# Optimization experiments

Hardware: AMD Instinct MI355X
Metric: run time of the kernel (lower is better)

## Reference

```python
import jax, jax.numpy as jnp
import numpy as np
from math import sqrt

B, N, CS, H, D, K = 8, 256, 512, 8, 64, 32
NB = 2 * K + 1          # no_bins = 65
CT = 2048               # c_transition
INF = 1e9
WL = sqrt(0.5)          # w_L
EPS = 1e-5


def setup_inputs() -> dict:
    key = jax.random.key(0)
    ks = jax.random.split(key, 10)
    sc = 0.02
    return {
        "s": jax.random.normal(ks[0], (B, N, CS), jnp.float32),
        "masks": jnp.ones((B, N), jnp.bool_),
        "wq": jax.random.normal(ks[1], (CS, D * H), jnp.float32) * sc,
        "wk": jax.random.normal(ks[2], (CS, D * H), jnp.float32) * sc,
        "wv": jax.random.normal(ks[3], (CS, D * H), jnp.float32) * sc,
        "wb": jax.random.normal(ks[4], (NB, H), jnp.float32) * sc,
        "wo": jax.random.normal(ks[5], ((NB + D) * H, CS), jnp.float32) * sc,
        "bo": jnp.zeros((CS,), jnp.float32),
        "ln1_g": jnp.ones((CS,), jnp.float32),
        "ln1_b": jnp.zeros((CS,), jnp.float32),
        "w1": jax.random.normal(ks[6], (CS, CT), jnp.float32) * sc,
        "b1": jnp.zeros((CT,), jnp.float32),
        "w2": jax.random.normal(ks[7], (CT, CS), jnp.float32) * sc,
        "b2": jnp.zeros((CS,), jnp.float32),
        "ln2_g": jnp.ones((CS,), jnp.float32),
        "ln2_b": jnp.zeros((CS,), jnp.float32),
    }


def _layernorm(x, g, b):
    m = jnp.mean(x, -1, keepdims=True)
    v = jnp.var(x, -1, keepdims=True)
    return (x - m) * jax.lax.rsqrt(v + EPS) * g + b


def _heads(x):  # [B,N,D*H] -> [B,H,N,D]  (torch: reshape(B,N,D,H) then move H forward)
    return jnp.transpose(x.reshape(B, N, D, H), (0, 3, 1, 2))


def reference(s, masks, wq, wk, wv, wb, wo, bo, ln1_g, ln1_b, w1, b1, w2, b2, ln2_g, ln2_b):
    mf = masks.astype(s.dtype)                       # [B,N]
    sq = mf[:, :, None] * mf[:, None, :]             # [B,N,N]

    # relative position one-hot, clipped to [-K, K] -> [N,N,NB]
    r = jnp.arange(N)
    dmat = jnp.clip(r[:, None] - r[None, :], -K, K) + K
    relpos_base = jax.nn.one_hot(dmat, NB, dtype=s.dtype)
    relpos = relpos_base[None] * sq[..., None]       # [B,N,N,NB]

    b_bias = jnp.einsum('bijc,ch->bhij', relpos, wb)  # [B,H,N,N]

    q = _heads(s @ wq)                               # [B,H,N,D]
    k = _heads(s @ wk)
    v = _heads(s @ wv)

    logits = WL * (jnp.einsum('bhid,bhjd->bhij', q, k) / sqrt(D) + b_bias)
    logits = logits - INF * (1.0 - sq)[:, None]      # mask
    a = jax.nn.softmax(logits, axis=-1)              # [B,H,N,N]

    # pairwise aggregation and value aggregation (einsum avoids [B,H,N,N,NB] blowup)
    o_pair = jnp.einsum('bhij,bijc->bhic', a, relpos)  # [B,H,N,NB]
    o = jnp.einsum('bhij,bhjd->bhid', a, v)            # [B,H,N,D]

    op = jnp.transpose(o_pair, (0, 2, 1, 3)).reshape(B, N, H * NB)
    ov = jnp.transpose(o, (0, 2, 1, 3)).reshape(B, N, H * D)
    embd = jnp.concatenate([op, ov], axis=-1) @ wo + bo   # [B,N,CS]

    x = _layernorm(s + embd, ln1_g, ln1_b)
    ff = jax.nn.relu(x @ w1 + b1) @ w2 + b2
    x = _layernorm(x + ff, ln2_g, ln2_b)
    return x, a
```

## Files before the change

### kernel.cpp

```cpp
#include <hip/hip_runtime.h>
#include <hip/hip_bf16.h>
#include <cstdint>

#define B_ 8
#define N_ 256
#define CS_ 512
#define H_ 8
#define D_ 64
#define K_ 32
#define NB_ 65
#define CT_ 2048
#define WL_ 0.70710678118654752f

typedef __attribute__((ext_vector_type(8))) short bf16x8;
typedef __attribute__((ext_vector_type(4))) float f32x4;

#define GLOBAL_AS __attribute__((address_space(1)))
#define LDS_AS __attribute__((address_space(3)))

__device__ __forceinline__ void async16(void* lds, const void* g) {
  __builtin_amdgcn_global_load_lds((const GLOBAL_AS uint32_t*)g,
                                   (LDS_AS uint32_t*)lds, 16, 0, 0);
}

__device__ __forceinline__ ushort f2bf(float v) {
  __hip_bfloat16 hb = __float2bfloat16(v);
  return *(ushort*)&hb;
}

__device__ __forceinline__ float bf2f(ushort u) {
  union { uint32_t ui; float f; } cv; cv.ui = (uint32_t)u << 16;
  return cv.f;
}

__global__ __launch_bounds__(128, 2) void gemm_bf16(
    const ushort* __restrict__ A, const ushort* __restrict__ Bt,
    const float* __restrict__ bias, float* __restrict__ C,
    ushort* __restrict__ Cb, int M, int Nc, int Kd, int flags) {
  __shared__ ushort As[2][64 * 64];
  __shared__ ushort Bs[2][64 * 64];
  int tid = threadIdx.x;
  int bm = blockIdx.y * 64, bn = blockIdx.x * 64;
  int S = gridDim.z, z = blockIdx.z;
  int T = Kd >> 6;
  int it0 = (z * T) / S, it1 = ((z + 1) * T) / S;
  if (flags & 32) Cb += (size_t)z * M * Nc;
  int w = tid >> 6, l = tid & 63;
  int lm = l & 15, lq = l >> 4;
  int srow = tid >> 3;
  int sg = tid & 7;

  f32x4 acc[2][4];
#pragma unroll
  for (int i = 0; i < 2; ++i)
#pragma unroll
    for (int j = 0; j < 4; ++j) acc[i][j] = (f32x4){0.f, 0.f, 0.f, 0.f};

  {
    int k0 = it0 << 6;
#pragma unroll
    for (int r = 0; r < 4; ++r) {
      int row = r * 16 + srow;
      int gl = sg ^ (row & 7);
      async16(&As[0][row * 64 + sg * 8],
              A + (size_t)(bm + row) * Kd + k0 + gl * 8);
      async16(&Bs[0][row * 64 + sg * 8],
              Bt + (size_t)(bn + row) * Kd + k0 + gl * 8);
    }
  }
  for (int it = it0; it < it1; ++it) {
    int cur = (it - it0) & 1;
    __syncthreads();
    if (it + 1 < it1) {
      int nxt = cur ^ 1;
      int k0 = (it + 1) << 6;
#pragma unroll
      for (int r = 0; r < 4; ++r) {
        int row = r * 16 + srow;
        int gl = sg ^ (row & 7);
        async16(&As[nxt][row * 64 + sg * 8],
                A + (size_t)(bm + row) * Kd + k0 + gl * 8);
        async16(&Bs[nxt][row * 64 + sg * 8],
                Bt + (size_t)(bn + row) * Kd + k0 + gl * 8);
      }
    }
#pragma unroll
    for (int kk = 0; kk < 2; ++kk) {
      bf16x8 af[2], bfr[4];
#pragma unroll
      for (int i = 0; i < 2; ++i) {
        int ma = w * 32 + 16 * i + lm;
        af[i] = *(const bf16x8*)&As[cur][ma * 64 + ((kk * 4 + lq) ^ (ma & 7)) * 8];
      }
#pragma unroll
      for (int j = 0; j < 4; ++j) {
        int nb = 16 * j + lm;
        bfr[j] = *(const bf16x8*)&Bs[cur][nb * 64 + ((kk * 4 + lq) ^ (nb & 7)) * 8];
      }
#pragma unroll
      for (int i = 0; i < 2; ++i)
#pragma unroll
        for (int j = 0; j < 4; ++j)
          acc[i][j] = __builtin_amdgcn_mfma_f32_16x16x32_bf16(
              af[i], bfr[j], acc[i][j], 0, 0, 0);
    }
  }
  __syncthreads();

  int lr = l >> 3, lc = l & 7;
  ushort* Tb = &As[0][0] + w * 2048;

#pragma unroll
  for (int j = 0; j < 4; ++j) {
    float bv = ((flags & 1) && z == 0) ? bias[bn + 16 * j + lm] : 0.f;
#pragma unroll
    for (int i = 0; i < 2; ++i)
#pragma unroll
      for (int r = 0; r < 4; ++r) {
        float v = acc[i][j][r] + bv;
        if (flags & 2) v = fmaxf(v, 0.f);
        Tb[(16 * i + lq * 4 + r) * 64 + 16 * j + lm] = f2bf(v);
      }
  }
  __asm__ __volatile__("" ::: "memory");
#pragma unroll
  for (int p = 0; p < 4; ++p) {
    int rowL = p * 8 + lr;
    bf16x8 vv = *(const bf16x8*)&Tb[rowL * 64 + lc * 8];
    *(bf16x8*)(Cb + (size_t)(bm + w * 32 + rowL) * Nc + bn + lc * 8) = vv;
  }
}

__global__ __launch_bounds__(128, 2) void qkvT(
    const ushort* __restrict__ A, const ushort* __restrict__ Bt,
    ushort* __restrict__ Cb,
    const float* __restrict__ wo, const float* __restrict__ w1,
    const float* __restrict__ w2, ushort* __restrict__ wopT,
    ushort* __restrict__ w1T, ushort* __restrict__ w2T) {
  __shared__ __align__(16) ushort As[2][64 * 64];
  __shared__ ushort Bs[2][64 * 64];
  int blk = blockIdx.x, tid = threadIdx.x;

  if (blk >= 768) {
    float (*tile)[33] = (float(*)[33])&As[0][0];
    int t = blk - 768;
    const float* src; ushort* dst;
    int R, C, Kpad, tX, tIdx;
    if (t < 544)       { tIdx = t;        src = wo; dst = wopT; R = 1032; C = 512;  Kpad = 1088; tX = 16; }
    else if (t < 1568) { tIdx = t - 544;  src = w1; dst = w1T;  R = 512;  C = 2048; Kpad = 512;  tX = 64; }
    else               { tIdx = t - 1568; src = w2; dst = w2T;  R = 2048; C = 512;  Kpad = 2048; tX = 16; }
    int c0 = (tIdx % tX) * 32, r0 = (tIdx / tX) * 32;
    int tx = tid & 7, ty = tid >> 3;
#pragma unroll
    for (int yy = 0; yy < 32; yy += 16) {
      int r = r0 + yy + ty, c = c0 + tx * 4;
      float4 v = (r < R) ? *(const float4*)&src[(size_t)r * C + c]
                         : (float4){0.f, 0.f, 0.f, 0.f};
      tile[yy + ty][tx * 4 + 0] = v.x;
      tile[yy + ty][tx * 4 + 1] = v.y;
      tile[yy + ty][tx * 4 + 2] = v.z;
      tile[yy + ty][tx * 4 + 3] = v.w;
    }
    __syncthreads();
#pragma unroll
    for (int yy = 0; yy < 32; yy += 16) {
      int cc = c0 + yy + ty;
      int k = r0 + tx * 4;
      float a0 = tile[tx * 4 + 0][yy + ty];
      float a1 = tile[tx * 4 + 1][yy + ty];
      float a2 = tile[tx * 4 + 2][yy + ty];
      float a3 = tile[tx * 4 + 3][yy + ty];
      ushort pk[4] = {f2bf(a0), f2bf(a1), f2bf(a2), f2bf(a3)};
      *(uint2*)&dst[(size_t)cc * Kpad + k] = *(uint2*)pk;
    }
    return;
  }

  int bm = (blk / 24) * 64, bn = (blk % 24) * 64;
  const int Kd = 512, it1 = 8;
  int w = tid >> 6, l = tid & 63;
  int lm = l & 15, lq = l >> 4;
  int srow = tid >> 3;
  int sg = tid & 7;

  f32x4 acc[2][4];
#pragma unroll
  for (int i = 0; i < 2; ++i)
#pragma unroll
    for (int j = 0; j < 4; ++j) acc[i][j] = (f32x4){0.f, 0.f, 0.f, 0.f};

  {
#pragma unroll
    for (int r = 0; r < 4; ++r) {
      int row = r * 16 + srow;
      int gl = sg ^ (row & 7);
      async16(&As[0][row * 64 + sg * 8],
              A + (size_t)(bm + row) * Kd + gl * 8);
      async16(&Bs[0][row * 64 + sg * 8],
              Bt + (size_t)(bn + row) * Kd + gl * 8);
    }
  }
  for (int it = 0; it < it1; ++it) {
    int cur = it & 1;
    __syncthreads();
    if (it + 1 < it1) {
      int nxt = cur ^ 1;
      int k0 = (it + 1) << 6;
#pragma unroll
      for (int r = 0; r < 4; ++r) {
        int row = r * 16 + srow;
        int gl = sg ^ (row & 7);
        async16(&As[nxt][row * 64 + sg * 8],
                A + (size_t)(bm + row) * Kd + k0 + gl * 8);
        async16(&Bs[nxt][row * 64 + sg * 8],
                Bt + (size_t)(bn + row) * Kd + k0 + gl * 8);
      }
    }
#pragma unroll
    for (int kk = 0; kk < 2; ++kk) {
      bf16x8 af[2], bfr[4];
#pragma unroll
      for (int i = 0; i < 2; ++i) {
        int ma = w * 32 + 16 * i + lm;
        af[i] = *(const bf16x8*)&As[cur][ma * 64 + ((kk * 4 + lq) ^ (ma & 7)) * 8];
      }
#pragma unroll
      for (int j = 0; j < 4; ++j) {
        int nb = 16 * j + lm;
        bfr[j] = *(const bf16x8*)&Bs[cur][nb * 64 + ((kk * 4 + lq) ^ (nb & 7)) * 8];
      }
#pragma unroll
      for (int i = 0; i < 2; ++i)
#pragma unroll
        for (int j = 0; j < 4; ++j)
          acc[i][j] = __builtin_amdgcn_mfma_f32_16x16x32_bf16(
              af[i], bfr[j], acc[i][j], 0, 0, 0);
    }
  }
  __syncthreads();

  int lr = l >> 3, lc = l & 7;
  ushort* Tb = &As[0][0] + w * 2048;

  int which = bn >> 9;
  int hh = (bn & 511) >> 6;
  int b = bm >> 8, nn0 = bm & 255;
  if (which == 2) {
#pragma unroll
    for (int j = 0; j < 4; ++j)
#pragma unroll
      for (int i = 0; i < 2; ++i) {
        ushort pk[4];
#pragma unroll
        for (int r = 0; r < 4; ++r) pk[r] = f2bf(acc[i][j][r]);
        *(uint2*)&Tb[(16 * j + lm) * 32 + 16 * i + lq * 4] = *(uint2*)pk;
      }
  } else {
#pragma unroll
    for (int j = 0; j < 4; ++j)
#pragma unroll
      for (int i = 0; i < 2; ++i)
#pragma unroll
        for (int r = 0; r < 4; ++r)
          Tb[(16 * i + lq * 4 + r) * 64 + 16 * j + lm] = f2bf(acc[i][j][r]);
  }
  __asm__ __volatile__("" ::: "memory");
  ushort* dstb = Cb + (size_t)which * 1048576 + (size_t)(b * 8 + hh) * 16384;
  if (which == 2) {
    int vr = l >> 2, vc = l & 3;
#pragma unroll
    for (int p = 0; p < 4; ++p) {
      int rowL = p * 16 + vr;
      bf16x8 vv = *(const bf16x8*)&Tb[rowL * 32 + vc * 8];
      *(bf16x8*)(dstb + (size_t)rowL * 256 + nn0 + w * 32 + vc * 8) = vv;
    }
  } else {
#pragma unroll
    for (int p = 0; p < 4; ++p) {
      int rowL = p * 8 + lr;
      bf16x8 vv = *(const bf16x8*)&Tb[rowL * 64 + lc * 8];
      *(bf16x8*)(dstb + (size_t)(nn0 + w * 32 + rowL) * 64 + lc * 8) = vv;
    }
  }
}

__global__ __launch_bounds__(256) void prep_small(
    const float* __restrict__ s, __hip_bfloat16* __restrict__ s_bf,
    const float* __restrict__ wq, const float* __restrict__ wk,
    const float* __restrict__ wv, __hip_bfloat16* __restrict__ wqkvT) {
  int blk = blockIdx.x;
  if (blk < 512) {
    int i = blk * 256 + threadIdx.x;
    float4 a = ((const float4*)s)[i * 2];
    float4 c = ((const float4*)s)[i * 2 + 1];
    ushort pk[8] = {f2bf(a.x), f2bf(a.y), f2bf(a.z), f2bf(a.w),
                    f2bf(c.x), f2bf(c.y), f2bf(c.z), f2bf(c.w)};
    *(uint4*)&((ushort*)s_bf)[i * 8] = *(uint4*)pk;
    return;
  }
  int t = blk - 512;
  __shared__ float tile[32][33];
  int zz = t >> 8, tIdx = t & 255;
  const float* src = zz == 0 ? wq : zz == 1 ? wk : wv;
  int whichBase = zz * 512;
  int c0 = (tIdx & 15) * 32, r0 = (tIdx >> 4) * 32;
  int tx = threadIdx.x & 7, ty = threadIdx.x >> 3;
  {
    int r = r0 + ty, c = c0 + tx * 4;
    float4 v = *(const float4*)&src[(size_t)r * 512 + c];
    tile[ty][tx * 4 + 0] = v.x;
    tile[ty][tx * 4 + 1] = v.y;
    tile[ty][tx * 4 + 2] = v.z;
    tile[ty][tx * 4 + 3] = v.w;
  }
  __syncthreads();
  {
    int cc = c0 + ty;
    int k = r0 + tx * 4;
    float a0 = tile[tx * 4 + 0][ty];
    float a1 = tile[tx * 4 + 1][ty];
    float a2 = tile[tx * 4 + 2][ty];
    float a3 = tile[tx * 4 + 3][ty];
    int n = whichBase + (cc & 7) * 64 + (cc >> 3);
    ushort pk[4] = {f2bf(a0), f2bf(a1), f2bf(a2), f2bf(a3)};
    *(uint2*)&((ushort*)wqkvT)[(size_t)n * 512 + k] = *(uint2*)pk;
  }
}

__global__ __launch_bounds__(128) void attn_fused(
    const ushort* __restrict__ qh, const ushort* __restrict__ kh,
    const ushort* __restrict__ vT, const int* __restrict__ masks,
    const float* __restrict__ wb, float* __restrict__ a_out,
    ushort* __restrict__ cat) {
  int strip = blockIdx.x & 7, bh = blockIdx.x >> 3;
  int h = bh & 7, b = bh >> 3;
  __shared__ ushort Ks[256 * 64];
  __shared__ ushort Ps[32 * 64];
  __shared__ float wbs[NB_];
  __shared__ float mfj[256];
  int tid = threadIdx.x;
  int srow = tid >> 3, sg = tid & 7;
#pragma unroll
  for (int rr = 0; rr < 16; ++rr) {
    int row = rr * 16 + srow;
    int gl = sg ^ (row & 7);
    async16(&Ks[row * 64 + sg * 8],
            kh + ((size_t)bh * 256 + row) * 64 + gl * 8);
  }
  int w = tid >> 6, l = tid & 63, lm = l & 15, lq = l >> 4;
  bf16x8 qf[2];
  {
    const ushort* qrow =
        qh + ((size_t)bh * 256 + strip * 32 + w * 16 + lm) * 64 + lq * 8;
    qf[0] = *(const bf16x8*)qrow;
    qf[1] = *(const bf16x8*)(qrow + 32);
  }
  if (tid < NB_) wbs[tid] = wb[tid * H_ + h];
  mfj[tid]       = (masks[b * 256 + tid] != 0) ? 1.f : 0.f;
  mfj[tid + 128] = (masks[b * 256 + tid + 128] != 0) ? 1.f : 0.f;
  __syncthreads();

  f32x4 acc[16];
#pragma unroll
  for (int ct = 0; ct < 16; ++ct) {
    int krow = ct * 16 + lm;
    bf16x8 kf0 = *(const bf16x8*)&Ks[krow * 64 + ((lq) ^ (krow & 7)) * 8];
    bf16x8 kf1 = *(const bf16x8*)&Ks[krow * 64 + ((4 + lq) ^ (krow & 7)) * 8];
    f32x4 zf = (f32x4){0.f, 0.f, 0.f, 0.f};
    zf = __builtin_amdgcn_mfma_f32_16x16x32_bf16(qf[0], kf0, zf, 0, 0, 0);
    acc[ct] = __builtin_amdgcn_mfma_f32_16x16x32_bf16(qf[1], kf1, zf, 0, 0, 0);
  }
  int ibase = strip * 32 + w * 16 + lq * 4;
  float mfi[4];
#pragma unroll
  for (int r = 0; r < 4; ++r) mfi[r] = mfj[ibase + r];
#pragma unroll
  for (int ct = 0; ct < 16; ++ct) {
    int j = ct * 16 + lm;
    float mj = mfj[j];
#pragma unroll
    for (int r = 0; r < 4; ++r) {
      int i = ibase + r;
      int diff = i - j;
      int cb = diff < -K_ ? 0 : (diff > K_ ? 2 * K_ : diff + K_);
      float sq = mfi[r] * mj;
      acc[ct][r] = WL_ * (acc[ct][r] * 0.125f + wbs[cb] * sq) - 1e9f * (1.f - sq);
    }
  }
  float mx[4], sm[4];
#pragma unroll
  for (int r = 0; r < 4; ++r) {
    float m = acc[0][r];
#pragma unroll
    for (int ct = 1; ct < 16; ++ct) m = fmaxf(m, acc[ct][r]);
#pragma unroll
    for (int o = 1; o < 16; o <<= 1) m = fmaxf(m, __shfl_xor(m, o, 64));
    mx[r] = m;
  }
#pragma unroll
  for (int ct = 0; ct < 16; ++ct)
#pragma unroll
    for (int r = 0; r < 4; ++r) acc[ct][r] = __expf(acc[ct][r] - mx[r]);
#pragma unroll
  for (int r = 0; r < 4; ++r) {
    float s = 0.f;
#pragma unroll
    for (int ct = 0; ct < 16; ++ct) s += acc[ct][r];
#pragma unroll
    for (int o = 1; o < 16; o <<= 1) s += __shfl_xor(s, o, 64);
    sm[r] = 1.f / s;
  }
  float p0[4] = {0.f, 0.f, 0.f, 0.f}, p64[4] = {0.f, 0.f, 0.f, 0.f};
#pragma unroll
  for (int ct = 0; ct < 16; ++ct) {
    int j = ct * 16 + lm;
    float mj = mfj[j];
#pragma unroll
    for (int r = 0; r < 4; ++r) {
      int i = ibase + r;
      float aval = acc[ct][r] * sm[r];
      a_out[((size_t)bh * 256 + i) * 256 + j] = aval;
      float val = aval * mfi[r] * mj;
      int diff = i - j;
      if (diff <= -K_)      p0[r] += val;
      else if (diff >= K_)  p64[r] += val;
      else cat[((size_t)(b * 256 + i)) * 1088 + h * 65 + diff + K_] = f2bf(val);
    }
  }
#pragma unroll
  for (int r = 0; r < 4; ++r)
#pragma unroll
    for (int o = 1; o < 16; o <<= 1) {
      p0[r]  += __shfl_xor(p0[r], o, 64);
      p64[r] += __shfl_xor(p64[r], o, 64);
    }
  if (lm == 0) {
#pragma unroll
    for (int r = 0; r < 4; ++r) {
      int i = ibase + r;
      cat[((size_t)(b * 256 + i)) * 1088 + h * 65 + 0]      = f2bf(p0[r]);
      cat[((size_t)(b * 256 + i)) * 1088 + h * 65 + 2 * K_] = f2bf(p64[r]);
    }
  }
#pragma unroll
  for (int r = 0; r < 4; ++r) {
    int i = ibase + r;
#pragma unroll
    for (int t = 0; t < 4; ++t) {
      int c = 1 + lm + 16 * t;
      if (c < 64) {
        int j = i - c + K_;
        if (j < 0 || j > 255)
          cat[((size_t)(b * 256 + i)) * 1088 + h * 65 + c] = 0;
      }
    }
  }
  if (h == 0) {
    for (int idx = tid; idx < 32 * 56; idx += 128) {
      int r = idx / 56, c = 1032 + (idx - r * 56);
      cat[((size_t)(b * 256 + strip * 32 + r)) * 1088 + c] = 0;
    }
  }
  f32x4 acc2[4];
#pragma unroll
  for (int nt = 0; nt < 4; ++nt) acc2[nt] = (f32x4){0.f, 0.f, 0.f, 0.f};
  const ushort* vbase = vT + (size_t)bh * 16384;
#pragma unroll
  for (int qt = 0; qt < 4; ++qt) {
    bf16x8 vf0[4], vf1[4];
#pragma unroll
    for (int nt = 0; nt < 4; ++nt) {
      const ushort* vrow = vbase + (size_t)(nt * 16 + lm) * 256 + qt * 64 + lq * 8;
      vf0[nt] = *(const bf16x8*)vrow;
      vf1[nt] = *(const bf16x8*)(vrow + 32);
    }
#pragma unroll
    for (int ctl = 0; ctl < 4; ++ctl) {
      int ct = qt * 4 + ctl;
#pragma unroll
      for (int r = 0; r < 4; ++r) {
        int rowl = w * 16 + lq * 4 + r;
        int g = ctl * 2 + (lm >> 3);
        Ps[rowl * 64 + ((g ^ (rowl & 7)) << 3) + (lm & 7)] =
            f2bf(acc[ct][r] * sm[r]);
      }
    }
    int prow = w * 16 + lm;
#pragma unroll
    for (int kst = 0; kst < 2; ++kst) {
      bf16x8 af = *(const bf16x8*)&Ps[prow * 64 + (((kst * 4 + lq) ^ (prow & 7)) << 3)];
#pragma unroll
      for (int nt = 0; nt < 4; ++nt)
        acc2[nt] = __builtin_amdgcn_mfma_f32_16x16x32_bf16(
            af, kst ? vf1[nt] : vf0[nt], acc2[nt], 0, 0, 0);
    }
  }
#pragma unroll
  for (int nt = 0; nt < 4; ++nt) {
    int d = nt * 16 + lm;
#pragma unroll
    for (int r = 0; r < 4; ++r) {
      int i = ibase + r;
      cat[((size_t)(b * 256 + i)) * 1088 + 520 + h * 64 + d] = f2bf(acc2[nt][r]);
    }
  }
}

__global__ __launch_bounds__(128) void ln_sum(
    const float* __restrict__ x1, const ushort* __restrict__ xp,
    int S, int stride, const float* __restrict__ g,
    const float* __restrict__ bta, float* __restrict__ out,
    __hip_bfloat16* __restrict__ out_bf) {
  __shared__ float redA[2], redB[2];
  int row = blockIdx.x, tid = threadIdx.x;
  size_t base = (size_t)row * 512;
  float4 v = *(const float4*)(x1 + base + tid * 4);
  for (int s = 0; s < S; ++s) {
    uint2 p = *(const uint2*)(xp + (size_t)s * stride + base + tid * 4);
    v.x += bf2f((ushort)(p.x & 0xffff));
    v.y += bf2f((ushort)(p.x >> 16));
    v.z += bf2f((ushort)(p.y & 0xffff));
    v.w += bf2f((ushort)(p.y >> 16));
  }
  float su = v.x + v.y + v.z + v.w;
  float sq = v.x * v.x + v.y * v.y + v.z * v.z + v.w * v.w;
#pragma unroll
  for (int o = 32; o > 0; o >>= 1) {
    su += __shfl_xor(su, o, 64);
    sq += __shfl_xor(sq, o, 64);
  }
  int w = tid >> 6;
  if ((tid & 63) == 0) { redA[w] = su; redB[w] = sq; }
  __syncthreads();
  su = redA[0] + redA[1]; sq = redB[0] + redB[1];
  float mean = su * (1.f / 512.f);
  float var = sq * (1.f / 512.f) - mean * mean;
  float inv = rsqrtf(var + 1e-5f);
  float4 gv = *(const float4*)(g + tid * 4);
  float4 bv = *(const float4*)(bta + tid * 4);
  float4 o4;
  o4.x = (v.x - mean) * inv * gv.x + bv.x;
  o4.y = (v.y - mean) * inv * gv.y + bv.y;
  o4.z = (v.z - mean) * inv * gv.z + bv.z;
  o4.w = (v.w - mean) * inv * gv.w + bv.w;
  *(float4*)(out + base + tid * 4) = o4;
  if (out_bf) {
    ushort pk[4] = {f2bf(o4.x), f2bf(o4.y), f2bf(o4.z), f2bf(o4.w)};
    *(uint2*)&((ushort*)out_bf)[base + tid * 4] = *(uint2*)pk;
  }
}

extern "C" void kernel_launch(void* const* d_in, const int* in_sizes, int n_in,
                              void* d_out, int out_size, void* d_ws, size_t ws_size,
                              hipStream_t stream) {
  const float* s     = (const float*)d_in[0];
  const int*   masks = (const int*)d_in[1];
  const float* wq = (const float*)d_in[2];
  const float* wk = (const float*)d_in[3];
  const float* wv = (const float*)d_in[4];
  const float* wb = (const float*)d_in[5];
  const float* wo = (const float*)d_in[6];
  const float* bo = (const float*)d_in[7];
  const float* ln1_g = (const float*)d_in[8];
  const float* ln1_b = (const float*)d_in[9];
  const float* w1 = (const float*)d_in[10];
  const float* b1 = (const float*)d_in[11];
  const float* w2 = (const float*)d_in[12];
  const float* b2 = (const float*)d_in[13];
  const float* ln2_g = (const float*)d_in[14];
  const float* ln2_b = (const float*)d_in[15];

  float* out_x = (float*)d_out;
  float* out_a = out_x + 1048576;

  float* ws = (float*)d_ws;
  ushort* embd_part = (ushort*)(ws + 0);
  float* xbuf       = ws + 4194304;
  ushort* ff_part   = (ushort*)(ws + 5242880);
  ushort* qkv_bf    = (ushort*)(ws + 9437184);
  ushort* q_bf = qkv_bf;
  ushort* k_bf = qkv_bf + 1048576;
  ushort* v_bf = qkv_bf + 2097152;
  ushort* cat_bf = (ushort*)(ws + 10223616);
  __hip_bfloat16* h_bf  = (__hip_bfloat16*)(ws + 11337728);
  __hip_bfloat16* s_bf  = (__hip_bfloat16*)(ws + 13434880);
  __hip_bfloat16* x_bf  = (__hip_bfloat16*)(ws + 13959168);
  __hip_bfloat16* wqkvT = (__hip_bfloat16*)(ws + 14483456);
  ushort* wopT  = (ushort*)(ws + 14876672);
  ushort* w1T   = (ushort*)(ws + 15155200);
  ushort* w2T   = (ushort*)(ws + 15679488);

  dim3 blkg(128);
  prep_small<<<dim3(1280), dim3(256), 0, stream>>>(s, s_bf, wq, wk, wv, wqkvT);
  qkvT<<<dim3(3360), blkg, 0, stream>>>(
      (const ushort*)s_bf, (const ushort*)wqkvT, qkv_bf,
      wo, w1, w2, wopT, w1T, w2T);
  attn_fused<<<dim3(512), blkg, 0, stream>>>(q_bf, k_bf, v_bf, masks, wb,
                                             out_a, cat_bf);
  gemm_bf16<<<dim3(8, 32, 2), blkg, 0, stream>>>(
      cat_bf, wopT, bo, nullptr, embd_part, 2048, 512, 1088, 1 | 4 | 32);
  ln_sum<<<dim3(2048), blkg, 0, stream>>>(s, embd_part, 2, 1048576,
                                          ln1_g, ln1_b, xbuf, x_bf);
  gemm_bf16<<<dim3(32, 32, 1), blkg, 0, stream>>>(
      (const ushort*)x_bf, w1T, b1, nullptr, (ushort*)h_bf,
      2048, 2048, 512, 1 | 2 | 4);
  gemm_bf16<<<dim3(8, 32, 2), blkg, 0, stream>>>(
      (const ushort*)h_bf, w2T, b2, nullptr, ff_part,
      2048, 512, 2048, 1 | 4 | 32);
  ln_sum<<<dim3(2048), blkg, 0, stream>>>(xbuf, ff_part, 2, 1048576,
                                          ln2_g, ln2_b, out_x, nullptr);
}
```

Before: 169.3 us.

## Convert fp32 weights to bf16 inside GEMM B-staging instead of separate transpose pass

Drops the pre-pass that transposed and converted wo, w1 and w2 to bf16 inside the qkv kernel. The GEMM now reads the fp32 weights directly in row-major order into registers, converts and packs pairs of k values into bf16, and writes them into the swizzled LDS B tile. The register prefetch for the next tile overlaps the MFMA loop. This removes one full read and write of the weights plus the extra blocks, but the GEMMs now read twice as many weight bytes per tile and do the conversion work in the inner loop.

```diff
diff --git a/kernel.cpp b/kernel.cpp
--- a/kernel.cpp
+++ b/kernel.cpp
@@ -33,10 +33,10 @@
   return cv.f;
 }
 
-__global__ __launch_bounds__(128, 2) void gemm_bf16(
-    const ushort* __restrict__ A, const ushort* __restrict__ Bt,
-    const float* __restrict__ bias, float* __restrict__ C,
-    ushort* __restrict__ Cb, int M, int Nc, int Kd, int flags) {
+__global__ __launch_bounds__(128, 2) void gemm_wf32(
+    const ushort* __restrict__ A, const float* __restrict__ W,
+    const float* __restrict__ bias, ushort* __restrict__ Cb,
+    int M, int Nc, int Kd, int Kw, int flags) {
   __shared__ ushort As[2][64 * 64];
   __shared__ ushort Bs[2][64 * 64];
   int tid = threadIdx.x;
@@ -47,8 +47,8 @@
   if (flags & 32) Cb += (size_t)z * M * Nc;
   int w = tid >> 6, l = tid & 63;
   int lm = l & 15, lq = l >> 4;
-  int srow = tid >> 3;
-  int sg = tid & 7;
+  int srow = tid >> 3, sg = tid & 7;
+  int n4 = tid & 15, kpr = tid >> 4;
 
   f32x4 acc[2][4];
 #pragma unroll
@@ -56,33 +56,56 @@
 #pragma unroll
     for (int j = 0; j < 4; ++j) acc[i][j] = (f32x4){0.f, 0.f, 0.f, 0.f};
 
-  {
-    int k0 = it0 << 6;
-#pragma unroll
-    for (int r = 0; r < 4; ++r) {
-      int row = r * 16 + srow;
-      int gl = sg ^ (row & 7);
-      async16(&As[0][row * 64 + sg * 8],
-              A + (size_t)(bm + row) * Kd + k0 + gl * 8);
-      async16(&Bs[0][row * 64 + sg * 8],
-              Bt + (size_t)(bn + row) * Kd + k0 + gl * 8);
-    }
-  }
+  float4 br0[4], br1[4];
+#define STAGE_A(buf, itx)                                                    \
+  {                                                                          \
+    int k0 = (itx) << 6;                                                     \
+    _Pragma("unroll") for (int r = 0; r < 4; ++r) {                          \
+      int row = r * 16 + srow;                                               \
+      int gl = sg ^ (row & 7);                                               \
+      async16(&As[buf][row * 64 + sg * 8],                                   \
+              A + (size_t)(bm + row) * Kd + k0 + gl * 8);                    \
+    }                                                                        \
+  }
+#define LOAD_B(itx)                                                          \
+  {                                                                          \
+    int k0 = (itx) << 6;                                                     \
+    _Pragma("unroll") for (int r = 0; r < 4; ++r) {                          \
+      int kp = kpr + r * 8;                                                  \
+      int k = k0 + 2 * kp;                                                   \
+      const float* p = W + (size_t)k * Nc + bn + n4 * 4;                     \
+      br0[r] = (k < Kw) ? *(const float4*)p : (float4){0.f, 0.f, 0.f, 0.f};  \
+      br1[r] = (k + 1 < Kw) ? *(const float4*)(p + Nc)                       \
+                            : (float4){0.f, 0.f, 0.f, 0.f};                  \
+    }                                                                        \
+  }
+#define WRITE_B(buf)                                                         \
+  {                                                                          \
+    _Pragma("unroll") for (int r = 0; r < 4; ++r) {                          \
+      int kp = kpr + r * 8;                                                  \
+      int kg = kp >> 2;                                                      \
+      _Pragma("unroll") for (int i = 0; i < 4; ++i) {                        \
+        int n = n4 * 4 + i;                                                  \
+        uint32_t v = (uint32_t)f2bf(((const float*)&br0[r])[i]) |            \
+                     ((uint32_t)f2bf(((const float*)&br1[r])[i]) << 16);     \
+        *(uint32_t*)((char*)&Bs[buf][0] + n * 128 +                          \
+                     ((kg ^ (n & 7)) << 4) + (kp & 3) * 4) = v;              \
+      }                                                                      \
+    }                                                                        \
+  }
+
+  STAGE_A(0, it0);
+  LOAD_B(it0);
+  WRITE_B(0);
+
   for (int it = it0; it < it1; ++it) {
     int cur = (it - it0) & 1;
+    int nxt = cur ^ 1;
     __syncthreads();
-    if (it + 1 < it1) {
-      int nxt = cur ^ 1;
-      int k0 = (it + 1) << 6;
-#pragma unroll
-      for (int r = 0; r < 4; ++r) {
-        int row = r * 16 + srow;
-        int gl = sg ^ (row & 7);
-        async16(&As[nxt][row * 64 + sg * 8],
-                A + (size_t)(bm + row) * Kd + k0 + gl * 8);
-        async16(&Bs[nxt][row * 64 + sg * 8],
-                Bt + (size_t)(bn + row) * Kd + k0 + gl * 8);
-      }
+    bool pf = (it + 1 < it1);
+    if (pf) {
+      STAGE_A(nxt, it + 1);
+      LOAD_B(it + 1);
     }
 #pragma unroll
     for (int kk = 0; kk < 2; ++kk) {
@@ -104,6 +127,7 @@
           acc[i][j] = __builtin_amdgcn_mfma_f32_16x16x32_bf16(
               af[i], bfr[j], acc[i][j], 0, 0, 0);
     }
+    if (pf) WRITE_B(nxt);
   }
   __syncthreads();
 
@@ -129,53 +153,17 @@
     bf16x8 vv = *(const bf16x8*)&Tb[rowL * 64 + lc * 8];
     *(bf16x8*)(Cb + (size_t)(bm + w * 32 + rowL) * Nc + bn + lc * 8) = vv;
   }
-}
-
-__global__ __launch_bounds__(128, 2) void qkvT(
+#undef STAGE_A
+#undef LOAD_B
+#undef WRITE_B
+}
+
+__global__ __launch_bounds__(128, 2) void qkv_gemm(
     const ushort* __restrict__ A, const ushort* __restrict__ Bt,
-    ushort* __restrict__ Cb,
-    const float* __restrict__ wo, const float* __restrict__ w1,
-    const float* __restrict__ w2, ushort* __restrict__ wopT,
-    ushort* __restrict__ w1T, ushort* __restrict__ w2T) {
+    ushort* __restrict__ Cb) {
   __shared__ __align__(16) ushort As[2][64 * 64];
   __shared__ ushort Bs[2][64 * 64];
   int blk = blockIdx.x, tid = threadIdx.x;
-
-  if (blk >= 768) {
-    float (*tile)[33] = (float(*)[33])&As[0][0];
-    int t = blk - 768;
-    const float* src; ushort* dst;
-    int R, C, Kpad, tX, tIdx;
-    if (t < 544)       { tIdx = t;        src = wo; dst = wopT; R = 1032; C = 512;  Kpad = 1088; tX = 16; }
-    else if (t < 1568) { tIdx = t - 544;  src = w1; dst = w1T;  R = 512;  C = 2048; Kpad = 512;  tX = 64; }
-    else               { tIdx = t - 1568; src = w2; dst = w2T;  R = 2048; C = 512;  Kpad = 2048; tX = 16; }
-    int c0 = (tIdx % tX) * 32, r0 = (tIdx / tX) * 32;
-    int tx = tid & 7, ty = tid >> 3;
-#pragma unroll
-    for (int yy = 0; yy < 32; yy += 16) {
-      int r = r0 + yy + ty, c = c0 + tx * 4;
-      float4 v = (r < R) ? *(const float4*)&src[(size_t)r * C + c]
-                         : (float4){0.f, 0.f, 0.f, 0.f};
-      tile[yy + ty][tx * 4 + 0] = v.x;
-      tile[yy + ty][tx * 4 + 1] = v.y;
-      tile[yy + ty][tx * 4 + 2] = v.z;
-      tile[yy + ty][tx * 4 + 3] = v.w;
-    }
-    __syncthreads();
-#pragma unroll
-    for (int yy = 0; yy < 32; yy += 16) {
-      int cc = c0 + yy + ty;
-      int k = r0 + tx * 4;
-      float a0 = tile[tx * 4 + 0][yy + ty];
-      float a1 = tile[tx * 4 + 1][yy + ty];
-      float a2 = tile[tx * 4 + 2][yy + ty];
-      float a3 = tile[tx * 4 + 3][yy + ty];
-      ushort pk[4] = {f2bf(a0), f2bf(a1), f2bf(a2), f2bf(a3)};
-      *(uint2*)&dst[(size_t)cc * Kpad + k] = *(uint2*)pk;
-    }
-    return;
-  }
-
   int bm = (blk / 24) * 64, bn = (blk % 24) * 64;
   const int Kd = 512, it1 = 8;
   int w = tid >> 6, l = tid & 63;
@@ -586,27 +574,21 @@
   __hip_bfloat16* s_bf  = (__hip_bfloat16*)(ws + 13434880);
   __hip_bfloat16* x_bf  = (__hip_bfloat16*)(ws + 13959168);
   __hip_bfloat16* wqkvT = (__hip_bfloat16*)(ws + 14483456);
-  ushort* wopT  = (ushort*)(ws + 14876672);
-  ushort* w1T   = (ushort*)(ws + 15155200);
-  ushort* w2T   = (ushort*)(ws + 15679488);
 
   dim3 blkg(128);
   prep_small<<<dim3(1280), dim3(256), 0, stream>>>(s, s_bf, wq, wk, wv, wqkvT);
-  qkvT<<<dim3(3360), blkg, 0, stream>>>(
-      (const ushort*)s_bf, (const ushort*)wqkvT, qkv_bf,
-      wo, w1, w2, wopT, w1T, w2T);
+  qkv_gemm<<<dim3(768), blkg, 0, stream>>>(
+      (const ushort*)s_bf, (const ushort*)wqkvT, qkv_bf);
   attn_fused<<<dim3(512), blkg, 0, stream>>>(q_bf, k_bf, v_bf, masks, wb,
                                              out_a, cat_bf);
-  gemm_bf16<<<dim3(8, 32, 2), blkg, 0, stream>>>(
-      cat_bf, wopT, bo, nullptr, embd_part, 2048, 512, 1088, 1 | 4 | 32);
+  gemm_wf32<<<dim3(8, 32, 2), blkg, 0, stream>>>(
+      cat_bf, wo, bo, embd_part, 2048, 512, 1088, 1032, 1 | 32);
   ln_sum<<<dim3(2048), blkg, 0, stream>>>(s, embd_part, 2, 1048576,
                                           ln1_g, ln1_b, xbuf, x_bf);
-  gemm_bf16<<<dim3(32, 32, 1), blkg, 0, stream>>>(
-      (const ushort*)x_bf, w1T, b1, nullptr, (ushort*)h_bf,
-      2048, 2048, 512, 1 | 2 | 4);
-  gemm_bf16<<<dim3(8, 32, 2), blkg, 0, stream>>>(
-      (const ushort*)h_bf, w2T, b2, nullptr, ff_part,
-      2048, 512, 2048, 1 | 4 | 32);
+  gemm_wf32<<<dim3(32, 32, 1), blkg, 0, stream>>>(
+      (const ushort*)x_bf, w1, b1, (ushort*)h_bf, 2048, 2048, 512, 512, 1 | 2);
+  gemm_wf32<<<dim3(8, 32, 2), blkg, 0, stream>>>(
+      (const ushort*)h_bf, w2, b2, ff_part, 2048, 512, 2048, 2048, 1 | 32);
   ln_sum<<<dim3(2048), blkg, 0, stream>>>(xbuf, ff_part, 2, 1048576,
                                           ln2_g, ln2_b, out_x, nullptr);
 }
```

New measurement: 192.5 us. 1.14x slower.
